# Performance work log

Measured on AMD Instinct MI355X. Metric: run time of the kernel, lower is better.

Reference implementation:

```python
import jax, jax.numpy as jnp
import numpy as np

R, C, N, E = 1, 4, 10000, 160000
H, EF, L, OUT = 128, 16, 3, 64


def _gelu(v):
    # torch F.gelu default = exact erf gelu
    return jax.nn.gelu(v, approximate=False)


def setup_inputs() -> dict:
    key = jax.random.key(0)
    ks = jax.random.split(key, 16)
    s = 0.05
    return {
        "x": jax.random.normal(ks[0], (R, C, N, H), jnp.float32),
        "node_mask": jax.random.uniform(ks[1], (R, C, N, 1), jnp.float32),
        "edge_attr": jax.random.normal(ks[2], (E, EF), jnp.float32),
        "bondW": jax.random.normal(ks[3], (EF, H), jnp.float32) * s,
        "bondb": jnp.zeros((H,), jnp.float32),
        "convW1": jax.random.normal(ks[4], (L, H, H), jnp.float32) * s,
        "convb1": jnp.zeros((L, H), jnp.float32),
        "convW2": jax.random.normal(ks[5], (L, H, H), jnp.float32) * s,
        "convb2": jnp.zeros((L, H), jnp.float32),
        "eps": jnp.zeros((L,), jnp.float32),
        "mlpW1": jax.random.normal(ks[6], (H, H), jnp.float32) * s,
        "mlpb1": jnp.zeros((H,), jnp.float32),
        "mlpW2": jax.random.normal(ks[7], (H, OUT), jnp.float32) * s,
        "mlpb2": jnp.zeros((OUT,), jnp.float32),
        "edge_index": jax.random.randint(ks[8], (2, E), 0, N, jnp.int32),
        "batch": jnp.zeros((N,), jnp.int32),
    }


def reference(x, node_mask, edge_attr, bondW, bondb, convW1, convb1, convW2, convb2,
              eps, mlpW1, mlpb1, mlpW2, mlpb2, edge_index, batch):
    src, dst = edge_index[0], edge_index[1]
    # shared bond encoder (Linear), broadcast to [1,1,E,H]
    edge_emb = edge_attr @ bondW + bondb                      # [E, H]
    # edge_weight = node_mask gathered at both endpoints      # [R, C, E, 1]
    edge_mask = node_mask[:, :, src, :] * node_mask[:, :, dst, :]
    for l in range(L):
        # gather-add-GELU-weight-scatter message passing
        msg = _gelu(x[:, :, src, :] + edge_emb) * edge_mask   # [R, C, E, H]
        agg = jnp.zeros_like(x).at[:, :, dst, :].add(msg)     # scatter_sum over dst
        h = (1.0 + eps[l]) * x + agg
        # conv mlp: Linear -> GELU -> Linear
        h = _gelu(h @ convW1[l] + convb1[l]) @ convW2[l] + convb2[l]
        h = _gelu(h)  # outer activation (norm=Identity, dropout=0)
        x = x + h     # residual
    # final MLP (num_mlp_layers=2, PyG MLP default relu act)
    y = jax.nn.relu(x @ mlpW1 + mlpb1) @ mlpW2 + mlpb2        # [R, C, N, OUT]
    denom = jax.lax.stop_gradient(node_mask).sum(axis=2)      # [R, C, 1]
    out = (y * node_mask).sum(axis=2) / denom                 # [R, C, OUT]
    return out
```

## Files before the change

### kernel.cpp

```cpp
#include <hip/hip_runtime.h>
#include <hip/hip_bf16.h>
#include <cstddef>
#include <cstdint>

#define NNODES 10000
#define NEDGES 160000
#define NH     128
#define NCOMBO 4
#define NMROWS (NCOMBO * NNODES)
#define FTILE  32
#define SSTR   136
#define FTILES (NMROWS / FTILE)

typedef __attribute__((ext_vector_type(8))) short short8v;
typedef __attribute__((ext_vector_type(4))) float f32x4;

__device__ __forceinline__ float gelu_f(float v) {
    const float u  = v * 0.70710678118654752f;
    float au = __builtin_fabsf(u);
    au = fminf(au, 3.9192f);
    const float t  = __builtin_amdgcn_rcpf(__builtin_fmaf(0.3275911f, au, 1.0f));
    const float e  = __builtin_amdgcn_exp2f(au * au * -1.4426950408889634f);
    float p = __builtin_fmaf(1.061405429f, t, -1.453152027f);
    p = __builtin_fmaf(p, t, 1.421413741f);
    p = __builtin_fmaf(p, t, -0.284496736f);
    p = __builtin_fmaf(p, t, 0.254829592f);
    const float erf_abs = 1.0f - p * t * e;
    const float erf_s   = __builtin_copysignf(erf_abs, v);
    return 0.5f * v * (1.0f + erf_s);
}

__device__ __forceinline__ uint16_t f2bf_rne(float f) {
    const uint32_t x = __float_as_uint(f);
    return (uint16_t)((x + 0x7fffu + ((x >> 16) & 1u)) >> 16);
}
__device__ __forceinline__ uint32_t packbf2(float lo, float hi) {
    return ((uint32_t)f2bf_rne(hi) << 16) | (uint32_t)f2bf_rne(lo);
}
__device__ __forceinline__ float bflo(uint32_t u) { return __uint_as_float(u << 16); }
__device__ __forceinline__ float bfhi(uint32_t u) { return __uint_as_float(u & 0xffff0000u); }

__global__ __launch_bounds__(256) void hist_kernel(const int* __restrict__ ei,
                                                   int* __restrict__ deg) {
    const int e = blockIdx.x * 256 + threadIdx.x;
    if (e < NEDGES) atomicAdd(&deg[ei[NEDGES + e]], 1);
}

__global__ __launch_bounds__(1024) void scan_kernel(const int* __restrict__ deg,
                                                    int* __restrict__ off,
                                                    int* __restrict__ cursor) {
    __shared__ int ssum[1024];
    const int tid  = threadIdx.x;
    const int base = tid * 10;
    int loc[10];
    int s = 0;
    #pragma unroll
    for (int i = 0; i < 10; ++i) {
        const int idx = base + i;
        loc[i] = s;
        s += (idx < NNODES) ? deg[idx] : 0;
    }
    ssum[tid] = s;
    for (int d = 1; d < 1024; d <<= 1) {
        __syncthreads();
        const int t = (tid >= d) ? ssum[tid - d] : 0;
        __syncthreads();
        ssum[tid] += t;
    }
    __syncthreads();
    const int pref = ssum[tid] - s;
    #pragma unroll
    for (int i = 0; i < 10; ++i) {
        const int idx = base + i;
        if (idx < NNODES) { off[idx] = pref + loc[i]; cursor[idx] = pref + loc[i]; }
    }
    if (tid == 0) off[NNODES] = NEDGES;
}

__global__ __launch_bounds__(256) void scatter_kernel(const int* __restrict__ ei,
                                                      const float* __restrict__ ea,
                                                      int* __restrict__ cursor,
                                                      int* __restrict__ esrc,
                                                      float* __restrict__ ea_s) {
    const int e = blockIdx.x * 256 + threadIdx.x;
    if (e < NEDGES) {
        const int src = ei[e];
        const int dst = ei[NEDGES + e];
        const int pos = atomicAdd(&cursor[dst], 1);
        esrc[pos] = src;
        const float4* s = reinterpret_cast<const float4*>(ea + (size_t)e * 16);
        float4*       d = reinterpret_cast<float4*>(ea_s + (size_t)pos * 16);
        d[0] = s[0]; d[1] = s[1]; d[2] = s[2]; d[3] = s[3];
    }
}

__global__ __launch_bounds__(256) void emb_kernel(
    const float* __restrict__ ea_s, const float* __restrict__ bW,
    const float* __restrict__ bb, uint32_t* __restrict__ embq)
{
    const int lane = threadIdx.x & 63;
    const int wid  = threadIdx.x >> 6;
    const int c0   = lane * 2;
    float2 wc[16];
    #pragma unroll
    for (int k = 0; k < 16; ++k)
        wc[k] = *reinterpret_cast<const float2*>(&bW[k * 128 + c0]);
    const float2 bbr = *reinterpret_cast<const float2*>(&bb[c0]);

    for (int j = blockIdx.x * 4 + wid; j < NEDGES; j += gridDim.x * 4) {
        const float4* eap = reinterpret_cast<const float4*>(ea_s + (size_t)j * 16);
        const float4 a0 = eap[0], a1 = eap[1], a2 = eap[2], a3 = eap[3];
        float s0 = bbr.x, s1 = bbr.y;
        s0 += a0.x*wc[0].x + a0.y*wc[1].x + a0.z*wc[2].x + a0.w*wc[3].x
            + a1.x*wc[4].x + a1.y*wc[5].x + a1.z*wc[6].x + a1.w*wc[7].x
            + a2.x*wc[8].x + a2.y*wc[9].x + a2.z*wc[10].x + a2.w*wc[11].x
            + a3.x*wc[12].x + a3.y*wc[13].x + a3.z*wc[14].x + a3.w*wc[15].x;
        s1 += a0.x*wc[0].y + a0.y*wc[1].y + a0.z*wc[2].y + a0.w*wc[3].y
            + a1.x*wc[4].y + a1.y*wc[5].y + a1.z*wc[6].y + a1.w*wc[7].y
            + a2.x*wc[8].y + a2.y*wc[9].y + a2.z*wc[10].y + a2.w*wc[11].y
            + a3.x*wc[12].y + a3.y*wc[13].y + a3.z*wc[14].y + a3.w*wc[15].y;
        embq[(size_t)j * 64 + lane] = packbf2(s0, s1);
    }
}

__global__ __launch_bounds__(256) void wtrans_kernel(
    const float* __restrict__ cW1, const float* __restrict__ cW2,
    const float* __restrict__ mW1, const float* __restrict__ mW2,
    short* __restrict__ wbf)
{
    const int gidx = blockIdx.x * 256 + threadIdx.x;
    if (gidx >= 122880) return;
    if (gidx < 114688) {
        const int m  = gidx >> 14;
        const int el = gidx & 16383;
        const int n  = el >> 7;
        const int k  = el & 127;
        const float* W = (m < 3) ? (cW1 + m * 16384)
                       : (m < 6) ? (cW2 + (m - 3) * 16384) : mW1;
        wbf[(size_t)m * 16384 + n * 128 + k] = (short)f2bf_rne(W[k * 128 + n]);
    } else {
        const int el = gidx - 114688;
        const int n  = el >> 7;
        const int k  = el & 127;
        wbf[114688 + n * 128 + k] = (short)f2bf_rne(mW2[k * 64 + n]);
    }
}

__global__ __launch_bounds__(256) void xcast_kernel(const float* __restrict__ x,
                                                    uint32_t* __restrict__ xbf) {
    const int i = blockIdx.x * 256 + threadIdx.x;
    if (i < NMROWS * 64) {
        const float2 v = *reinterpret_cast<const float2*>(&x[(size_t)i * 2]);
        xbf[i] = packbf2(v.x, v.y);
    }
}

__global__ __launch_bounds__(256) void agg2_kernel(
    const uint32_t* __restrict__ xbf,
    const float* __restrict__ nm,
    const uint32_t* __restrict__ embq,
    const int*   __restrict__ off,
    const int*   __restrict__ esrc,
    const float* __restrict__ epsp, int layer,
    uint32_t* __restrict__ hbf)
{
    const int lane = threadIdx.x & 63;
    const int wid  = threadIdx.x >> 6;
    const float epv = 1.0f + epsp[layer];

    for (int n = blockIdx.x * 4 + wid; n < NNODES; n += gridDim.x * 4) {
        const int j0 = off[n], j1 = off[n + 1];
        float dm[4];
        #pragma unroll
        for (int c = 0; c < 4; ++c) dm[c] = nm[c * NNODES + n];

        float acc[4][2] = {{0.f,0.f},{0.f,0.f},{0.f,0.f},{0.f,0.f}};

        uint32_t eq_c = 0; float mv_c[4]; uint32_t xu_c[4];
        if (j0 < j1) {
            const int s = esrc[j0];
            eq_c = embq[(size_t)j0 * 64 + lane];
            #pragma unroll
            for (int c = 0; c < 4; ++c) {
                mv_c[c] = nm[c * NNODES + s] * dm[c];
                xu_c[c] = xbf[((size_t)c * NNODES + s) * 64 + lane];
            }
        }
        for (int j = j0; j < j1; ++j) {
            const uint32_t eq = eq_c;
            float mv[4]; uint32_t xu[4];
            #pragma unroll
            for (int c = 0; c < 4; ++c) { mv[c] = mv_c[c]; xu[c] = xu_c[c]; }
            if (j + 1 < j1) {
                const int s = esrc[j + 1];
                eq_c = embq[(size_t)(j + 1) * 64 + lane];
                #pragma unroll
                for (int c = 0; c < 4; ++c) {
                    mv_c[c] = nm[c * NNODES + s] * dm[c];
                    xu_c[c] = xbf[((size_t)c * NNODES + s) * 64 + lane];
                }
            }
            const float e0 = bflo(eq);
            const float e1 = bfhi(eq);
            #pragma unroll
            for (int c = 0; c < 4; ++c) {
                acc[c][0] += gelu_f(bflo(xu[c]) + e0) * mv[c];
                acc[c][1] += gelu_f(bfhi(xu[c]) + e1) * mv[c];
            }
        }
        #pragma unroll
        for (int c = 0; c < 4; ++c) {
            const uint32_t u = xbf[((size_t)c * NNODES + n) * 64 + lane];
            const float o0 = epv * bflo(u) + acc[c][0];
            const float o1 = epv * bfhi(u) + acc[c][1];
            hbf[((size_t)c * NNODES + n) * 64 + lane] = packbf2(o0, o1);
        }
    }
}

__global__ __launch_bounds__(256) void agg_kernel(
    const float* __restrict__ xcur, const float* __restrict__ nm,
    const float* __restrict__ ea_s, const float* __restrict__ bW,
    const float* __restrict__ bb, const int* __restrict__ off,
    const int* __restrict__ esrc, const float* __restrict__ epsp, int layer,
    short* __restrict__ hbf_s)
{
    const int tid = threadIdx.x;
    const int h   = tid & 127;
    const int sub = tid >> 7;
    float wc[16];
    #pragma unroll
    for (int k = 0; k < 16; ++k) wc[k] = bW[k * 128 + h];
    const float bbr = bb[h];
    const float epv = 1.0f + epsp[layer];

    for (int n = blockIdx.x * 2 + sub; n < NNODES; n += gridDim.x * 2) {
        float acc0 = 0.f, acc1 = 0.f, acc2 = 0.f, acc3 = 0.f;
        const int j0 = off[n], j1 = off[n + 1];
        const float d0 = nm[0*NNODES+n], d1 = nm[1*NNODES+n];
        const float d2 = nm[2*NNODES+n], d3 = nm[3*NNODES+n];
        for (int j = j0; j < j1; ++j) {
            const int src = esrc[j];
            const float4* eap = reinterpret_cast<const float4*>(ea_s + (size_t)j * 16);
            const float4 a0 = eap[0], a1 = eap[1], a2 = eap[2], a3 = eap[3];
            float emb = bbr;
            emb += a0.x*wc[0] + a0.y*wc[1] + a0.z*wc[2] + a0.w*wc[3];
            emb += a1.x*wc[4] + a1.y*wc[5] + a1.z*wc[6] + a1.w*wc[7];
            emb += a2.x*wc[8] + a2.y*wc[9] + a2.z*wc[10] + a2.w*wc[11];
            emb += a3.x*wc[12] + a3.y*wc[13] + a3.z*wc[14] + a3.w*wc[15];
            const float m0 = nm[0*NNODES+src]*d0, m1 = nm[1*NNODES+src]*d1;
            const float m2 = nm[2*NNODES+src]*d2, m3 = nm[3*NNODES+src]*d3;
            acc0 += gelu_f(xcur[((size_t)0*NNODES+src)*NH+h] + emb) * m0;
            acc1 += gelu_f(xcur[((size_t)1*NNODES+src)*NH+h] + emb) * m1;
            acc2 += gelu_f(xcur[((size_t)2*NNODES+src)*NH+h] + emb) * m2;
            acc3 += gelu_f(xcur[((size_t)3*NNODES+src)*NH+h] + emb) * m3;
        }
        hbf_s[((size_t)0*NNODES+n)*NH+h] = (short)f2bf_rne(epv * xcur[((size_t)0*NNODES+n)*NH+h] + acc0);
        hbf_s[((size_t)1*NNODES+n)*NH+h] = (short)f2bf_rne(epv * xcur[((size_t)1*NNODES+n)*NH+h] + acc1);
        hbf_s[((size_t)2*NNODES+n)*NH+h] = (short)f2bf_rne(epv * xcur[((size_t)2*NNODES+n)*NH+h] + acc2);
        hbf_s[((size_t)3*NNODES+n)*NH+h] = (short)f2bf_rne(epv * xcur[((size_t)3*NNODES+n)*NH+h] + acc3);
    }
}

__global__ __launch_bounds__(256) void conv_mfma_kernel(
    const uint32_t* __restrict__ hb,
    const float* __restrict__ resid,
    const short* __restrict__ W1t, const float* __restrict__ b1,
    const short* __restrict__ W2t, const float* __restrict__ b2,
    float* __restrict__ outp,
    short* __restrict__ xb_s)
{
    __shared__ short sh[FTILE * SSTR];
    __shared__ short st[FTILE * SSTR];
    __shared__ short sw[128 * SSTR];

    const int tid  = threadIdx.x;
    const int lane = tid & 63;
    const int w    = tid >> 6;
    const int l15  = lane & 15;
    const int l4   = lane >> 4;
    const int colb = w * 32;
    const int row0 = blockIdx.x * FTILE;

    for (int i = tid; i < FTILE * 16; i += 256) {
        const int r = i >> 4, c = i & 15;
        *reinterpret_cast<uint4*>(&sh[r * SSTR + c * 8]) =
            *reinterpret_cast<const uint4*>(&hb[(size_t)(row0 + r) * 64 + c * 4]);
    }
    for (int i = tid; i < 128 * 16; i += 256) {
        const int r = i >> 4, c = i & 15;
        *reinterpret_cast<uint4*>(&sw[r * SSTR + c * 8]) =
            *reinterpret_cast<const uint4*>(&W1t[r * 128 + c * 8]);
    }
    __syncthreads();

    f32x4 a00 = {0,0,0,0}, a01 = {0,0,0,0}, a10 = {0,0,0,0}, a11 = {0,0,0,0};
    #pragma unroll
    for (int s = 0; s < 4; ++s) {
        const int ko = s * 32 + l4 * 8;
        short8v fa0 = *reinterpret_cast<const short8v*>(&sh[(l15)      * SSTR + ko]);
        short8v fa1 = *reinterpret_cast<const short8v*>(&sh[(16 + l15) * SSTR + ko]);
        short8v fb0 = *reinterpret_cast<const short8v*>(&sw[(colb + l15)      * SSTR + ko]);
        short8v fb1 = *reinterpret_cast<const short8v*>(&sw[(colb + 16 + l15) * SSTR + ko]);
        a00 = __builtin_amdgcn_mfma_f32_16x16x32_bf16(fa0, fb0, a00, 0, 0, 0);
        a01 = __builtin_amdgcn_mfma_f32_16x16x32_bf16(fa0, fb1, a01, 0, 0, 0);
        a10 = __builtin_amdgcn_mfma_f32_16x16x32_bf16(fa1, fb0, a10, 0, 0, 0);
        a11 = __builtin_amdgcn_mfma_f32_16x16x32_bf16(fa1, fb1, a11, 0, 0, 0);
    }

    {
        const float bv0 = b1[colb + l15];
        const float bv1 = b1[colb + 16 + l15];
        #pragma unroll
        for (int j = 0; j < 4; ++j) {
            const int r0 = l4 * 4 + j;
            st[r0 * SSTR + colb + l15]             = (short)f2bf_rne(gelu_f(a00[j] + bv0));
            st[r0 * SSTR + colb + 16 + l15]        = (short)f2bf_rne(gelu_f(a01[j] + bv1));
            st[(16 + r0) * SSTR + colb + l15]      = (short)f2bf_rne(gelu_f(a10[j] + bv0));
            st[(16 + r0) * SSTR + colb + 16 + l15] = (short)f2bf_rne(gelu_f(a11[j] + bv1));
        }
    }
    __syncthreads();

    for (int i = tid; i < 128 * 16; i += 256) {
        const int r = i >> 4, c = i & 15;
        *reinterpret_cast<uint4*>(&sw[r * SSTR + c * 8]) =
            *reinterpret_cast<const uint4*>(&W2t[r * 128 + c * 8]);
    }
    __syncthreads();

    a00 = {0,0,0,0}; a01 = {0,0,0,0}; a10 = {0,0,0,0}; a11 = {0,0,0,0};
    #pragma unroll
    for (int s = 0; s < 4; ++s) {
        const int ko = s * 32 + l4 * 8;
        short8v fa0 = *reinterpret_cast<const short8v*>(&st[(l15)      * SSTR + ko]);
        short8v fa1 = *reinterpret_cast<const short8v*>(&st[(16 + l15) * SSTR + ko]);
        short8v fb0 = *reinterpret_cast<const short8v*>(&sw[(colb + l15)      * SSTR + ko]);
        short8v fb1 = *reinterpret_cast<const short8v*>(&sw[(colb + 16 + l15) * SSTR + ko]);
        a00 = __builtin_amdgcn_mfma_f32_16x16x32_bf16(fa0, fb0, a00, 0, 0, 0);
        a01 = __builtin_amdgcn_mfma_f32_16x16x32_bf16(fa0, fb1, a01, 0, 0, 0);
        a10 = __builtin_amdgcn_mfma_f32_16x16x32_bf16(fa1, fb0, a10, 0, 0, 0);
        a11 = __builtin_amdgcn_mfma_f32_16x16x32_bf16(fa1, fb1, a11, 0, 0, 0);
    }

    {
        const float bv0 = b2[colb + l15];
        const float bv1 = b2[colb + 16 + l15];
        #pragma unroll
        for (int j = 0; j < 4; ++j) {
            const int r0 = row0 + l4 * 4 + j;
            const int r1 = r0 + 16;
            const size_t o00 = (size_t)r0 * NH + colb + l15;
            const size_t o01 = (size_t)r0 * NH + colb + 16 + l15;
            const size_t o10 = (size_t)r1 * NH + colb + l15;
            const size_t o11 = (size_t)r1 * NH + colb + 16 + l15;
            const float v00 = resid[o00] + gelu_f(a00[j] + bv0);
            const float v01 = resid[o01] + gelu_f(a01[j] + bv1);
            const float v10 = resid[o10] + gelu_f(a10[j] + bv0);
            const float v11 = resid[o11] + gelu_f(a11[j] + bv1);
            outp[o00] = v00; xb_s[o00] = (short)f2bf_rne(v00);
            outp[o01] = v01; xb_s[o01] = (short)f2bf_rne(v01);
            outp[o10] = v10; xb_s[o10] = (short)f2bf_rne(v10);
            outp[o11] = v11; xb_s[o11] = (short)f2bf_rne(v11);
        }
    }
}

__global__ __launch_bounds__(256) void mlp_mfma_kernel(
    const uint32_t* __restrict__ xb,
    const short* __restrict__ W1t, const float* __restrict__ b1,
    const short* __restrict__ W2t,
    const float* __restrict__ b2,
    const float* __restrict__ nm,
    float* __restrict__ oacc)
{
    __shared__ short sx[FTILE * SSTR];
    __shared__ short st[FTILE * SSTR];
    __shared__ short sw[128 * SSTR];
    __shared__ float sacc[256];

    const int tid  = threadIdx.x;
    const int lane = tid & 63;
    const int w    = tid >> 6;
    const int l15  = lane & 15;
    const int l4   = lane >> 4;
    const int colb = w * 32;
    const int row0 = blockIdx.x * FTILE;

    sacc[tid] = 0.0f;

    for (int i = tid; i < FTILE * 16; i += 256) {
        const int r = i >> 4, c = i & 15;
        *reinterpret_cast<uint4*>(&sx[r * SSTR + c * 8]) =
            *reinterpret_cast<const uint4*>(&xb[(size_t)(row0 + r) * 64 + c * 4]);
    }
    for (int i = tid; i < 128 * 16; i += 256) {
        const int r = i >> 4, c = i & 15;
        *reinterpret_cast<uint4*>(&sw[r * SSTR + c * 8]) =
            *reinterpret_cast<const uint4*>(&W1t[r * 128 + c * 8]);
    }
    __syncthreads();

    f32x4 a00 = {0,0,0,0}, a01 = {0,0,0,0}, a10 = {0,0,0,0}, a11 = {0,0,0,0};
    #pragma unroll
    for (int s = 0; s < 4; ++s) {
        const int ko = s * 32 + l4 * 8;
        short8v fa0 = *reinterpret_cast<const short8v*>(&sx[(l15)      * SSTR + ko]);
        short8v fa1 = *reinterpret_cast<const short8v*>(&sx[(16 + l15) * SSTR + ko]);
        short8v fb0 = *reinterpret_cast<const short8v*>(&sw[(colb + l15)      * SSTR + ko]);
        short8v fb1 = *reinterpret_cast<const short8v*>(&sw[(colb + 16 + l15) * SSTR + ko]);
        a00 = __builtin_amdgcn_mfma_f32_16x16x32_bf16(fa0, fb0, a00, 0, 0, 0);
        a01 = __builtin_amdgcn_mfma_f32_16x16x32_bf16(fa0, fb1, a01, 0, 0, 0);
        a10 = __builtin_amdgcn_mfma_f32_16x16x32_bf16(fa1, fb0, a10, 0, 0, 0);
        a11 = __builtin_amdgcn_mfma_f32_16x16x32_bf16(fa1, fb1, a11, 0, 0, 0);
    }

    {
        const float bv0 = b1[colb + l15];
        const float bv1 = b1[colb + 16 + l15];
        #pragma unroll
        for (int j = 0; j < 4; ++j) {
            const int r0 = l4 * 4 + j;
            st[r0 * SSTR + colb + l15]             = (short)f2bf_rne(fmaxf(a00[j] + bv0, 0.f));
            st[r0 * SSTR + colb + 16 + l15]        = (short)f2bf_rne(fmaxf(a01[j] + bv1, 0.f));
            st[(16 + r0) * SSTR + colb + l15]      = (short)f2bf_rne(fmaxf(a10[j] + bv0, 0.f));
            st[(16 + r0) * SSTR + colb + 16 + l15] = (short)f2bf_rne(fmaxf(a11[j] + bv1, 0.f));
        }
    }
    __syncthreads();

    for (int i = tid; i < 64 * 16; i += 256) {
        const int r = i >> 4, c = i & 15;
        *reinterpret_cast<uint4*>(&sw[r * SSTR + c * 8]) =
            *reinterpret_cast<const uint4*>(&W2t[r * 128 + c * 8]);
    }
    __syncthreads();

    const int colb2 = w * 16;
    f32x4 c0f = {0,0,0,0}, c1f = {0,0,0,0};
    #pragma unroll
    for (int s = 0; s < 4; ++s) {
        const int ko = s * 32 + l4 * 8;
        short8v fa0 = *reinterpret_cast<const short8v*>(&st[(l15)      * SSTR + ko]);
        short8v fa1 = *reinterpret_cast<const short8v*>(&st[(16 + l15) * SSTR + ko]);
        short8v fb  = *reinterpret_cast<const short8v*>(&sw[(colb2 + l15) * SSTR + ko]);
        c0f = __builtin_amdgcn_mfma_f32_16x16x32_bf16(fa0, fb, c0f, 0, 0, 0);
        c1f = __builtin_amdgcn_mfma_f32_16x16x32_bf16(fa1, fb, c1f, 0, 0, 0);
    }

    {
        const float bv = b2[colb2 + l15];
        #pragma unroll
        for (int j = 0; j < 4; ++j) {
            const int gr0 = row0 + l4 * 4 + j;
            const int gr1 = gr0 + 16;
            const float w0 = nm[gr0];
            const float w1 = nm[gr1];
            const int cb0 = gr0 / NNODES;
            const int cb1 = gr1 / NNODES;
            atomicAdd(&sacc[cb0 * 64 + colb2 + l15], (c0f[j] + bv) * w0);
            atomicAdd(&sacc[cb1 * 64 + colb2 + l15], (c1f[j] + bv) * w1);
        }
    }

    __syncthreads();
    atomicAdd(&oacc[tid], sacc[tid]);
}

__global__ __launch_bounds__(256) void final_kernel(
    const float* __restrict__ acc, const float* __restrict__ nm,
    float* __restrict__ outp)
{
    const int tid  = threadIdx.x;
    const int c    = tid >> 6;
    const int lane = tid & 63;
    float s = 0.f;
    for (int n = lane; n < NNODES; n += 64) s += nm[c * NNODES + n];
    #pragma unroll
    for (int off = 32; off > 0; off >>= 1) s += __shfl_down(s, off, 64);
    const float denom = __shfl(s, 0, 64);
    outp[tid] = acc[tid] / denom;
}

extern "C" void kernel_launch(void* const* d_in, const int* in_sizes, int n_in,
                              void* d_out, int out_size, void* d_ws, size_t ws_size,
                              hipStream_t stream) {
    const float* x    = (const float*)d_in[0];
    const float* nm   = (const float*)d_in[1];
    const float* ea   = (const float*)d_in[2];
    const float* bW   = (const float*)d_in[3];
    const float* bb   = (const float*)d_in[4];
    const float* cW1  = (const float*)d_in[5];
    const float* cb1  = (const float*)d_in[6];
    const float* cW2  = (const float*)d_in[7];
    const float* cb2  = (const float*)d_in[8];
    const float* eps  = (const float*)d_in[9];
    const float* mW1  = (const float*)d_in[10];
    const float* mb1  = (const float*)d_in[11];
    const float* mW2  = (const float*)d_in[12];
    const float* mb2  = (const float*)d_in[13];
    const int*   ei   = (const int*)d_in[14];

    float* ws = (float*)d_ws;
    const bool big = ws_size >= (size_t)23230600ULL * 4ULL;

    if (big) {
        float*    xcur = ws;
        float*    oacc = ws + 5120000;
        uint32_t* hbf  = (uint32_t*)(ws + 5120512);
        uint32_t* xbf  = (uint32_t*)(ws + 7680512);
        float*    ea_s = ws + 10240512;
        short*    wbf  = (short*)ea_s;
        uint32_t* embq = (uint32_t*)(ws + 12800512);
        int*      ib   = (int*)(ws + 23040512);
        int* off = ib; int* cur = ib + 10002; int* deg = ib + 20002;
        int* esrc = ib + 30002;

        hipMemsetAsync(deg, 0, 10000 * 4, stream);
        hist_kernel<<<(NEDGES + 255) / 256, 256, 0, stream>>>(ei, deg);
        scan_kernel<<<1, 1024, 0, stream>>>(deg, off, cur);
        scatter_kernel<<<(NEDGES + 255) / 256, 256, 0, stream>>>(ei, ea, cur, esrc, ea_s);
        emb_kernel<<<10000, 256, 0, stream>>>(ea_s, bW, bb, embq);
        wtrans_kernel<<<480, 256, 0, stream>>>(cW1, cW2, mW1, mW2, wbf);
        xcast_kernel<<<10000, 256, 0, stream>>>(x, xbf);

        for (int l = 0; l < 3; ++l) {
            const float* resid = (l == 0) ? x : xcur;
            agg2_kernel<<<2500, 256, 0, stream>>>(xbf, nm, embq, off, esrc, eps, l, hbf);
            conv_mfma_kernel<<<FTILES, 256, 0, stream>>>(hbf, resid,
                wbf + (size_t)l * 16384, cb1 + l * 128,
                wbf + (size_t)(3 + l) * 16384, cb2 + l * 128,
                xcur, (short*)xbf);
        }
        hipMemsetAsync(oacc, 0, 256 * 4, stream);
        mlp_mfma_kernel<<<FTILES, 256, 0, stream>>>(xbf, wbf + 98304, mb1,
                                                    wbf + 114688, mb2, nm, oacc);
        final_kernel<<<1, 256, 0, stream>>>(oacc, nm, (float*)d_out);
    } else {
        float*    xcur = ws;
        float*    oacc = ws + 5120000;
        uint32_t* hbf  = (uint32_t*)(ws + 5120512);
        uint32_t* xbf  = (uint32_t*)(ws + 7680512);
        float*    ea_s = ws + 10240512;
        int*      ib   = (int*)(ws + 12800512);
        int* off = ib; int* cur = ib + 10002; int* deg = ib + 20002;
        int* esrc = ib + 30002;
        short* wbf = (short*)(ib + 190004);

        hipMemcpyAsync(xcur, x, (size_t)5120000 * 4, hipMemcpyDeviceToDevice, stream);
        hipMemsetAsync(deg, 0, 10000 * 4, stream);
        hist_kernel<<<(NEDGES + 255) / 256, 256, 0, stream>>>(ei, deg);
        scan_kernel<<<1, 1024, 0, stream>>>(deg, off, cur);
        scatter_kernel<<<(NEDGES + 255) / 256, 256, 0, stream>>>(ei, ea, cur, esrc, ea_s);
        wtrans_kernel<<<480, 256, 0, stream>>>(cW1, cW2, mW1, mW2, wbf);

        for (int l = 0; l < 3; ++l) {
            agg_kernel<<<2500, 256, 0, stream>>>(xcur, nm, ea_s, bW, bb, off, esrc,
                                                 eps, l, (short*)hbf);
            conv_mfma_kernel<<<FTILES, 256, 0, stream>>>(hbf, xcur,
                wbf + (size_t)l * 16384, cb1 + l * 128,
                wbf + (size_t)(3 + l) * 16384, cb2 + l * 128,
                xcur, (short*)xbf);
        }
        hipMemsetAsync(oacc, 0, 256 * 4, stream);
        mlp_mfma_kernel<<<FTILES, 256, 0, stream>>>(xbf, wbf + 98304, mb1,
                                                    wbf + 114688, mb2, nm, oacc);
        final_kernel<<<1, 256, 0, stream>>>(oacc, nm, (float*)d_out);
    }
}
```

Measured before the change: 441.8 us.

## Interleave bf16 node features across combos and precompute per-edge masks

```diff
diff --git a/kernel.cpp b/kernel.cpp
--- a/kernel.cpp
+++ b/kernel.cpp
@@ -39,6 +39,10 @@
 }
 __device__ __forceinline__ float bflo(uint32_t u) { return __uint_as_float(u << 16); }
 __device__ __forceinline__ float bfhi(uint32_t u) { return __uint_as_float(u & 0xffff0000u); }
+
+__device__ __forceinline__ size_t xi2(int n, int ch, int c) {
+    return (size_t)n * 512 + (ch >> 1) * 8 + c * 2 + (ch & 1);
+}
 
 __global__ __launch_bounds__(256) void hist_kernel(const int* __restrict__ ei,
                                                    int* __restrict__ deg) {
@@ -146,19 +150,43 @@
     }
 }
 
+__global__ __launch_bounds__(256) void emsk_kernel(
+    const float* __restrict__ nm, const int* __restrict__ off,
+    const int* __restrict__ esrc, float4* __restrict__ emsk)
+{
+    const int n = blockIdx.x * 256 + threadIdx.x;
+    if (n >= NNODES) return;
+    const float d0 = nm[0 * NNODES + n], d1 = nm[1 * NNODES + n];
+    const float d2 = nm[2 * NNODES + n], d3 = nm[3 * NNODES + n];
+    const int j1 = off[n + 1];
+    for (int j = off[n]; j < j1; ++j) {
+        const int s = esrc[j];
+        emsk[j] = make_float4(nm[0 * NNODES + s] * d0, nm[1 * NNODES + s] * d1,
+                              nm[2 * NNODES + s] * d2, nm[3 * NNODES + s] * d3);
+    }
+}
+
 __global__ __launch_bounds__(256) void xcast_kernel(const float* __restrict__ x,
-                                                    uint32_t* __restrict__ xbf) {
+                                                    uint32_t* __restrict__ xbf2) {
     const int i = blockIdx.x * 256 + threadIdx.x;
-    if (i < NMROWS * 64) {
-        const float2 v = *reinterpret_cast<const float2*>(&x[(size_t)i * 2]);
-        xbf[i] = packbf2(v.x, v.y);
-    }
+    if (i >= NNODES * 64) return;
+    const int n = i >> 6, pair = i & 63;
+    uint4 o;
+    {
+        const float2 v0 = *reinterpret_cast<const float2*>(&x[((size_t)0 * NNODES + n) * NH + pair * 2]);
+        const float2 v1 = *reinterpret_cast<const float2*>(&x[((size_t)1 * NNODES + n) * NH + pair * 2]);
+        const float2 v2 = *reinterpret_cast<const float2*>(&x[((size_t)2 * NNODES + n) * NH + pair * 2]);
+        const float2 v3 = *reinterpret_cast<const float2*>(&x[((size_t)3 * NNODES + n) * NH + pair * 2]);
+        o.x = packbf2(v0.x, v0.y); o.y = packbf2(v1.x, v1.y);
+        o.z = packbf2(v2.x, v2.y); o.w = packbf2(v3.x, v3.y);
+    }
+    *reinterpret_cast<uint4*>(&xbf2[(size_t)i * 4]) = o;
 }
 
 __global__ __launch_bounds__(256) void agg2_kernel(
-    const uint32_t* __restrict__ xbf,
-    const float* __restrict__ nm,
+    const uint32_t* __restrict__ xbf2,
     const uint32_t* __restrict__ embq,
+    const float4* __restrict__ emsk,
     const int*   __restrict__ off,
     const int*   __restrict__ esrc,
     const float* __restrict__ epsp, int layer,
@@ -170,49 +198,41 @@
 
     for (int n = blockIdx.x * 4 + wid; n < NNODES; n += gridDim.x * 4) {
         const int j0 = off[n], j1 = off[n + 1];
-        float dm[4];
-        #pragma unroll
-        for (int c = 0; c < 4; ++c) dm[c] = nm[c * NNODES + n];
-
         float acc[4][2] = {{0.f,0.f},{0.f,0.f},{0.f,0.f},{0.f,0.f}};
 
-        uint32_t eq_c = 0; float mv_c[4]; uint32_t xu_c[4];
+        uint32_t eq_c = 0; uint4 xq_c = {0,0,0,0}; float4 em_c = {0,0,0,0};
         if (j0 < j1) {
             const int s = esrc[j0];
             eq_c = embq[(size_t)j0 * 64 + lane];
-            #pragma unroll
-            for (int c = 0; c < 4; ++c) {
-                mv_c[c] = nm[c * NNODES + s] * dm[c];
-                xu_c[c] = xbf[((size_t)c * NNODES + s) * 64 + lane];
-            }
+            xq_c = *reinterpret_cast<const uint4*>(&xbf2[((size_t)s * 64 + lane) * 4]);
+            em_c = emsk[j0];
         }
         for (int j = j0; j < j1; ++j) {
             const uint32_t eq = eq_c;
-            float mv[4]; uint32_t xu[4];
-            #pragma unroll
-            for (int c = 0; c < 4; ++c) { mv[c] = mv_c[c]; xu[c] = xu_c[c]; }
+            const uint4  xq = xq_c;
+            const float4 em = em_c;
             if (j + 1 < j1) {
                 const int s = esrc[j + 1];
                 eq_c = embq[(size_t)(j + 1) * 64 + lane];
-                #pragma unroll
-                for (int c = 0; c < 4; ++c) {
-                    mv_c[c] = nm[c * NNODES + s] * dm[c];
-                    xu_c[c] = xbf[((size_t)c * NNODES + s) * 64 + lane];
-                }
+                xq_c = *reinterpret_cast<const uint4*>(&xbf2[((size_t)s * 64 + lane) * 4]);
+                em_c = emsk[j + 1];
             }
             const float e0 = bflo(eq);
             const float e1 = bfhi(eq);
+            const uint32_t xs[4] = {xq.x, xq.y, xq.z, xq.w};
+            const float    ms[4] = {em.x, em.y, em.z, em.w};
             #pragma unroll
             for (int c = 0; c < 4; ++c) {
-                acc[c][0] += gelu_f(bflo(xu[c]) + e0) * mv[c];
-                acc[c][1] += gelu_f(bfhi(xu[c]) + e1) * mv[c];
+                acc[c][0] += gelu_f(bflo(xs[c]) + e0) * ms[c];
+                acc[c][1] += gelu_f(bfhi(xs[c]) + e1) * ms[c];
             }
         }
+        const uint4 xn = *reinterpret_cast<const uint4*>(&xbf2[((size_t)n * 64 + lane) * 4]);
+        const uint32_t xns[4] = {xn.x, xn.y, xn.z, xn.w};
         #pragma unroll
         for (int c = 0; c < 4; ++c) {
-            const uint32_t u = xbf[((size_t)c * NNODES + n) * 64 + lane];
-            const float o0 = epv * bflo(u) + acc[c][0];
-            const float o1 = epv * bfhi(u) + acc[c][1];
+            const float o0 = epv * bflo(xns[c]) + acc[c][0];
+            const float o1 = epv * bfhi(xns[c]) + acc[c][1];
             hbf[((size_t)c * NNODES + n) * 64 + lane] = packbf2(o0, o1);
         }
     }
@@ -268,7 +288,7 @@
     const short* __restrict__ W1t, const float* __restrict__ b1,
     const short* __restrict__ W2t, const float* __restrict__ b2,
     float* __restrict__ outp,
-    short* __restrict__ xb_s)
+    short* __restrict__ xb2)
 {
     __shared__ short sh[FTILE * SSTR];
     __shared__ short st[FTILE * SSTR];
@@ -346,28 +366,32 @@
     {
         const float bv0 = b2[colb + l15];
         const float bv1 = b2[colb + 16 + l15];
+        const int c00 = colb + l15;
+        const int c01 = colb + 16 + l15;
         #pragma unroll
         for (int j = 0; j < 4; ++j) {
             const int r0 = row0 + l4 * 4 + j;
             const int r1 = r0 + 16;
-            const size_t o00 = (size_t)r0 * NH + colb + l15;
-            const size_t o01 = (size_t)r0 * NH + colb + 16 + l15;
-            const size_t o10 = (size_t)r1 * NH + colb + l15;
-            const size_t o11 = (size_t)r1 * NH + colb + 16 + l15;
+            const int cb0 = r0 / NNODES, nn0 = r0 - cb0 * NNODES;
+            const int cb1 = r1 / NNODES, nn1 = r1 - cb1 * NNODES;
+            const size_t o00 = (size_t)r0 * NH + c00;
+            const size_t o01 = (size_t)r0 * NH + c01;
+            const size_t o10 = (size_t)r1 * NH + c00;
+            const size_t o11 = (size_t)r1 * NH + c01;
             const float v00 = resid[o00] + gelu_f(a00[j] + bv0);
             const float v01 = resid[o01] + gelu_f(a01[j] + bv1);
             const float v10 = resid[o10] + gelu_f(a10[j] + bv0);
             const float v11 = resid[o11] + gelu_f(a11[j] + bv1);
-            outp[o00] = v00; xb_s[o00] = (short)f2bf_rne(v00);
-            outp[o01] = v01; xb_s[o01] = (short)f2bf_rne(v01);
-            outp[o10] = v10; xb_s[o10] = (short)f2bf_rne(v10);
-            outp[o11] = v11; xb_s[o11] = (short)f2bf_rne(v11);
+            outp[o00] = v00; xb2[xi2(nn0, c00, cb0)] = (short)f2bf_rne(v00);
+            outp[o01] = v01; xb2[xi2(nn0, c01, cb0)] = (short)f2bf_rne(v01);
+            outp[o10] = v10; xb2[xi2(nn1, c00, cb1)] = (short)f2bf_rne(v10);
+            outp[o11] = v11; xb2[xi2(nn1, c01, cb1)] = (short)f2bf_rne(v11);
         }
     }
 }
 
 __global__ __launch_bounds__(256) void mlp_mfma_kernel(
-    const uint32_t* __restrict__ xb,
+    const float* __restrict__ x,
     const short* __restrict__ W1t, const float* __restrict__ b1,
     const short* __restrict__ W2t,
     const float* __restrict__ b2,
@@ -389,10 +413,13 @@
 
     sacc[tid] = 0.0f;
 
-    for (int i = tid; i < FTILE * 16; i += 256) {
-        const int r = i >> 4, c = i & 15;
-        *reinterpret_cast<uint4*>(&sx[r * SSTR + c * 8]) =
-            *reinterpret_cast<const uint4*>(&xb[(size_t)(row0 + r) * 64 + c * 4]);
+    for (int i = tid; i < FTILE * 32; i += 256) {
+        const int r = i >> 5, q = i & 31;
+        const float4 v = reinterpret_cast<const float4*>(x + (size_t)(row0 + r) * NH)[q];
+        uint2 pk;
+        pk.x = packbf2(v.x, v.y);
+        pk.y = packbf2(v.z, v.w);
+        *reinterpret_cast<uint2*>(&sx[r * SSTR + q * 4]) = pk;
     }
     for (int i = tid; i < 128 * 16; i += 256) {
         const int r = i >> 4, c = i & 15;
@@ -508,9 +535,10 @@
         float*    xcur = ws;
         float*    oacc = ws + 5120000;
         uint32_t* hbf  = (uint32_t*)(ws + 5120512);
-        uint32_t* xbf  = (uint32_t*)(ws + 7680512);
+        uint32_t* xbf2 = (uint32_t*)(ws + 7680512);
         float*    ea_s = ws + 10240512;
         short*    wbf  = (short*)ea_s;
+        float4*   emsk = (float4*)(ea_s + 61440);
         uint32_t* embq = (uint32_t*)(ws + 12800512);
         int*      ib   = (int*)(ws + 23040512);
         int* off = ib; int* cur = ib + 10002; int* deg = ib + 20002;
@@ -522,25 +550,27 @@
         scatter_kernel<<<(NEDGES + 255) / 256, 256, 0, stream>>>(ei, ea, cur, esrc, ea_s);
         emb_kernel<<<10000, 256, 0, stream>>>(ea_s, bW, bb, embq);
         wtrans_kernel<<<480, 256, 0, stream>>>(cW1, cW2, mW1, mW2, wbf);
-        xcast_kernel<<<10000, 256, 0, stream>>>(x, xbf);
+        emsk_kernel<<<(NNODES + 255) / 256, 256, 0, stream>>>(nm, off, esrc, emsk);
+        xcast_kernel<<<2500, 256, 0, stream>>>(x, xbf2);
 
         for (int l = 0; l < 3; ++l) {
             const float* resid = (l == 0) ? x : xcur;
-            agg2_kernel<<<2500, 256, 0, stream>>>(xbf, nm, embq, off, esrc, eps, l, hbf);
+            agg2_kernel<<<2500, 256, 0, stream>>>(xbf2, embq, emsk, off, esrc,
+                                                  eps, l, hbf);
             conv_mfma_kernel<<<FTILES, 256, 0, stream>>>(hbf, resid,
                 wbf + (size_t)l * 16384, cb1 + l * 128,
                 wbf + (size_t)(3 + l) * 16384, cb2 + l * 128,
-                xcur, (short*)xbf);
+                xcur, (short*)xbf2);
         }
         hipMemsetAsync(oacc, 0, 256 * 4, stream);
-        mlp_mfma_kernel<<<FTILES, 256, 0, stream>>>(xbf, wbf + 98304, mb1,
+        mlp_mfma_kernel<<<FTILES, 256, 0, stream>>>(xcur, wbf + 98304, mb1,
                                                     wbf + 114688, mb2, nm, oacc);
         final_kernel<<<1, 256, 0, stream>>>(oacc, nm, (float*)d_out);
     } else {
         float*    xcur = ws;
         float*    oacc = ws + 5120000;
         uint32_t* hbf  = (uint32_t*)(ws + 5120512);
-        uint32_t* xbf  = (uint32_t*)(ws + 7680512);
+        uint32_t* xbf2 = (uint32_t*)(ws + 7680512);
         float*    ea_s = ws + 10240512;
         int*      ib   = (int*)(ws + 12800512);
         int* off = ib; int* cur = ib + 10002; int* deg = ib + 20002;
@@ -555,15 +585,16 @@
         wtrans_kernel<<<480, 256, 0, stream>>>(cW1, cW2, mW1, mW2, wbf);
 
         for (int l = 0; l < 3; ++l) {
+            const float* resid = (l == 0) ? x : xcur;
             agg_kernel<<<2500, 256, 0, stream>>>(xcur, nm, ea_s, bW, bb, off, esrc,
                                                  eps, l, (short*)hbf);
-            conv_mfma_kernel<<<FTILES, 256, 0, stream>>>(hbf, xcur,
+            conv_mfma_kernel<<<FTILES, 256, 0, stream>>>(hbf, resid,
                 wbf + (size_t)l * 16384, cb1 + l * 128,
                 wbf + (size_t)(3 + l) * 16384, cb2 + l * 128,
-                xcur, (short*)xbf);
+                xcur, (short*)xbf2);
         }
         hipMemsetAsync(oacc, 0, 256 * 4, stream);
-        mlp_mfma_kernel<<<FTILES, 256, 0, stream>>>(xbf, wbf + 98304, mb1,
+        mlp_mfma_kernel<<<FTILES, 256, 0, stream>>>(xcur, wbf + 98304, mb1,
                                                     wbf + 114688, mb2, nm, oacc);
         final_kernel<<<1, 256, 0, stream>>>(oacc, nm, (float*)d_out);
     }
```

Measured after the change: 458.7 us. +3.8%, slower.
